# Optimization experiments

Measured on AMD Instinct MI355X. Metric: run time of the kernel, lower is better.

The kernel has to match this reference:

```python
import jax, jax.numpy as jnp
import numpy as np

NUM_BINS = 32
LAMBDA_W2 = 0.1
SMOOTHING = 1e-3
LABEL_SMOOTHING = 0.05


def setup_inputs() -> dict:
    key = jax.random.key(0)
    k1, k2, k3 = jax.random.split(key, 3)
    B, H, W = 64, 512, 512
    return {
        "changes_obs": jax.random.normal(k1, (B, H, W), dtype=jnp.float32),
        "changes_pred": jax.random.normal(k2, (B, H, W), dtype=jnp.float32),
        "mask": jax.random.randint(k3, (B, H, W), 0, 2).astype(bool),
        "bin_edges": jnp.linspace(-3.0, 3.0, NUM_BINS + 1, dtype=jnp.float32),
    }


def compute_histogram(changes, bin_edges, mask):
    # changes, mask: [B, H, W]; bin_edges: [num_bins+1]
    B = changes.shape[0]
    num_bins = bin_edges.shape[0] - 1
    x = changes.reshape(B, -1)                      # [B, N]
    m = mask.reshape(B, -1)                         # [B, N]
    # bucketize: bin i is [e_i, e_{i+1}), last bin closed on the right
    idx = jnp.searchsorted(bin_edges, x, side='right') - 1
    idx = jnp.clip(idx, 0, num_bins - 1)            # x == last edge -> last bin
    valid = m & (x >= bin_edges[0]) & (x <= bin_edges[-1])
    flat = (jnp.arange(B)[:, None] * num_bins + idx).reshape(-1)
    counts = jax.ops.segment_sum(
        valid.reshape(-1).astype(jnp.float32), flat, num_segments=B * num_bins
    ).reshape(B, num_bins)
    # torch: a sample with zero masked pixels gets counts of all ones
    n_masked = m.sum(axis=1)
    counts = jnp.where((n_masked == 0)[:, None], 1.0, counts)
    total = jnp.maximum(counts.sum(axis=1, keepdims=True), 1.0)
    proportions = counts / total
    return counts, proportions


def reference(changes_obs, changes_pred, mask, bin_edges):
    num_bins = bin_edges.shape[0] - 1
    _, p_obs = compute_histogram(changes_obs, bin_edges, mask)
    _, p_pred = compute_histogram(changes_pred, bin_edges, mask)
    p_pred = (1.0 - LABEL_SMOOTHING) * p_pred + LABEL_SMOOTHING / num_bins
    # class-balanced weights from observed proportions
    avg = p_obs.mean(axis=0)
    w = 1.0 / (avg + SMOOTHING)
    w = w * num_bins / w.sum()
    ce_loss = (-p_obs * jnp.log(p_pred + 1e-8) * w[None, :]).sum(axis=1).mean()
    # Wasserstein-2 on CDFs with midpoint-spacing bin widths
    mid = 0.5 * (bin_edges[:-1] + bin_edges[1:])
    bw = mid[1:] - mid[:-1]
    bw = jnp.concatenate([bw, bw[-1:]])
    cdf_obs = jnp.cumsum(p_obs, axis=1)
    cdf_pred = jnp.cumsum(p_pred, axis=1)
    w2_loss = (((cdf_obs - cdf_pred) ** 2) * bw[None, :]).sum(axis=1).mean()
    total_loss = (ce_loss + LAMBDA_W2 * w2_loss) / num_bins
    return total_loss, ce_loss, w2_loss, p_obs, p_pred
```

## Files before the change

### kernel.cpp

```cpp
#include <hip/hip_runtime.h>
#include <stdint.h>

#define NBINS 32
#define NBATCH 64
#define NPB (512 * 512)
#define BPB 32
#define TPB 256
#define EPB (NPB / BPB)
#define ITERS (EPB / (TPB * 4))

#define WS_PRED 2048
#define WS_NM   4096
#define WS_FLAG 4160
#define WS_WORDS 4161

__global__ void detect_mask_kernel(const uint32_t* __restrict__ mw,
                                   uint32_t* __restrict__ flag) {
  uint32_t v = mw[threadIdx.x];
  if (__any(v > 1u) && threadIdx.x == 0) *flag = 1u;
}

__device__ __forceinline__ int bin_of(float x) {
  float t = __builtin_fmaf(x, 5.333333492279053f, 16.0f);
  int i = (int)t;
  float fi = (float)i;
  float elo = __builtin_fmaf(fi, 0.1875f, -3.0f);
  float ehi = elo + 0.1875f;
  i += (x >= ehi) ? 1 : 0;
  i -= (x < elo) ? 1 : 0;
  return i;
}

__device__ __forceinline__ void count_one(int i, uint32_t h[8]) {
  const uint32_t inc = 1u << ((i & 3) << 3);
  const int hi = i >> 2;
#pragma unroll
  for (int r = 0; r < 8; ++r) h[r] += (hi == r) ? inc : 0u;
}

__global__ __launch_bounds__(TPB) void hist_kernel(
    const float* __restrict__ obs, const float* __restrict__ pred,
    const void* __restrict__ mask, uint32_t* __restrict__ ws) {
  __shared__ uint32_t red[4][32];

  const int tid = threadIdx.x;
  const uint32_t is_u8 = ws[WS_FLAG];
  const int b = blockIdx.x / BPB;
  const int chunk = blockIdx.x % BPB;
  const size_t base_f4 = (((size_t)b * NPB) + ((size_t)chunk * EPB)) >> 2;

  const float4* __restrict__ o4 = (const float4*)obs;
  const float4* __restrict__ p4 = (const float4*)pred;
  const uint32_t* __restrict__ mwp = (const uint32_t*)mask;
  const int4* __restrict__ mip = (const int4*)mask;

  uint32_t c[8] = {0, 0, 0, 0, 0, 0, 0, 0};
  uint32_t d[8] = {0, 0, 0, 0, 0, 0, 0, 0};
  uint32_t nm_pack = 0;
  uint32_t nm_cnt = 0;

#pragma unroll
  for (int it = 0; it < ITERS; ++it) {
    const size_t idx = base_f4 + (size_t)(it * TPB + tid);
    const float4 xo = o4[idx];
    const float4 xp = p4[idx];

    bool m0, m1, m2, m3;
    if (is_u8) {
      const uint32_t w = mwp[idx];
      nm_pack += w;
      m0 = (w & 0x000000ffu) != 0u;
      m1 = (w & 0x0000ff00u) != 0u;
      m2 = (w & 0x00ff0000u) != 0u;
      m3 = (w & 0xff000000u) != 0u;
    } else {
      const int4 mv = mip[idx];
      m0 = mv.x != 0; m1 = mv.y != 0; m2 = mv.z != 0; m3 = mv.w != 0;
      nm_cnt += (m0 ? 1u : 0u) + (m1 ? 1u : 0u) + (m2 ? 1u : 0u) + (m3 ? 1u : 0u);
    }

    const float a0 = m0 ? xo.x : 1e2f, b0 = m0 ? xp.x : 1e2f;
    const float a1 = m1 ? xo.y : 1e2f, b1 = m1 ? xp.y : 1e2f;
    const float a2 = m2 ? xo.z : 1e2f, b2 = m2 ? xp.z : 1e2f;
    const float a3 = m3 ? xo.w : 1e2f, b3 = m3 ? xp.w : 1e2f;

    count_one(bin_of(a0), c); count_one(bin_of(b0), d);
    count_one(bin_of(a1), c); count_one(bin_of(b1), d);
    count_one(bin_of(a2), c); count_one(bin_of(b2), d);
    count_one(bin_of(a3), c); count_one(bin_of(b3), d);
  }

  uint32_t nm = is_u8 ? ((nm_pack & 0xffu) + ((nm_pack >> 8) & 0xffu) +
                         ((nm_pack >> 16) & 0xffu) + (nm_pack >> 24))
                      : nm_cnt;
#pragma unroll
  for (int off = 32; off >= 1; off >>= 1) nm += __shfl_down(nm, off);
  if ((tid & 63) == 0) atomicAdd(&ws[WS_NM + b], nm);

#pragma unroll
  for (int m = 1; m <= 2; m <<= 1) {
#pragma unroll
    for (int r = 0; r < 8; ++r) {
      c[r] += __shfl_xor(c[r], m);
      d[r] += __shfl_xor(d[r], m);
    }
  }
  uint32_t cl[8], ch[8], dl[8], dh[8];
#pragma unroll
  for (int r = 0; r < 8; ++r) {
    cl[r] = c[r] & 0x00FF00FFu; ch[r] = (c[r] >> 8) & 0x00FF00FFu;
    dl[r] = d[r] & 0x00FF00FFu; dh[r] = (d[r] >> 8) & 0x00FF00FFu;
  }
#pragma unroll
  for (int m = 4; m <= 32; m <<= 1) {
#pragma unroll
    for (int r = 0; r < 8; ++r) {
      cl[r] += __shfl_xor(cl[r], m); ch[r] += __shfl_xor(ch[r], m);
      dl[r] += __shfl_xor(dl[r], m); dh[r] += __shfl_xor(dh[r], m);
    }
  }

  const int w = tid >> 6;
  if ((tid & 63) == 0) {
#pragma unroll
    for (int r = 0; r < 8; ++r) {
      red[w][r] = cl[r];
      red[w][8 + r] = ch[r];
      red[w][16 + r] = dl[r];
      red[w][24 + r] = dh[r];
    }
  }
  __syncthreads();

  if (tid < 2 * NBINS) {
    const int arr = tid >> 5;
    const int bin = tid & 31;
    const int slot = arr * 16 + (bin >> 2) + ((bin & 1) ? 8 : 0);
    const int shift = (bin & 2) ? 16 : 0;
    uint32_t s = 0;
#pragma unroll
    for (int wv = 0; wv < 4; ++wv) s += (red[wv][slot] >> shift) & 0xFFFFu;
    if (s) atomicAdd(&ws[(arr ? WS_PRED : 0) + b * NBINS + bin], s);
  }
}

__global__ __launch_bounds__(64) void finalize_kernel(
    const uint32_t* __restrict__ ws, const float* __restrict__ edges,
    float* __restrict__ out) {
  __shared__ float pobs[NBATCH][NBINS + 1];
  __shared__ float ppred[NBATCH][NBINS + 1];
  __shared__ float w_sh[NBINS];
  __shared__ float bw_sh[NBINS];
  __shared__ float w_scale;

  const int t = threadIdx.x;

  const uint32_t* co = ws + t * NBINS;
  const uint32_t* cp = ws + WS_PRED + t * NBINS;
  const uint32_t nmask = ws[WS_NM + t];

  float sum_o = 0.0f, sum_p = 0.0f;
#pragma unroll
  for (int j = 0; j < NBINS; ++j) {
    float vo = (nmask == 0u) ? 1.0f : (float)co[j];
    float vp = (nmask == 0u) ? 1.0f : (float)cp[j];
    pobs[t][j] = vo;  sum_o += vo;
    ppred[t][j] = vp; sum_p += vp;
  }
  const float inv_to = 1.0f / fmaxf(sum_o, 1.0f);
  const float inv_tp = 1.0f / fmaxf(sum_p, 1.0f);
#pragma unroll
  for (int j = 0; j < NBINS; ++j) {
    pobs[t][j] *= inv_to;
    ppred[t][j] = 0.95f * (ppred[t][j] * inv_tp) + 0.05f / (float)NBINS;
  }
  __syncthreads();

  if (t < NBINS) {
    float s = 0.0f;
#pragma unroll
    for (int b = 0; b < NBATCH; ++b) s += pobs[b][t];
    const float avg = s / (float)NBATCH;
    w_sh[t] = 1.0f / (avg + 1e-3f);
    const int j2 = (t < NBINS - 1) ? t : (NBINS - 2);
    const float mA = 0.5f * (edges[j2] + edges[j2 + 1]);
    const float mB = 0.5f * (edges[j2 + 1] + edges[j2 + 2]);
    bw_sh[t] = mB - mA;
  }
  __syncthreads();
  if (t == 0) {
    float sw = 0.0f;
#pragma unroll
    for (int j = 0; j < NBINS; ++j) sw += w_sh[j];
    w_scale = (float)NBINS / sw;
  }
  __syncthreads();

  float ce = 0.0f, w2 = 0.0f, cdf_o = 0.0f, cdf_p = 0.0f;
#pragma unroll
  for (int j = 0; j < NBINS; ++j) {
    const float po = pobs[t][j];
    const float pp = ppred[t][j];
    ce += -po * logf(pp + 1e-8f) * (w_sh[j] * w_scale);
    cdf_o += po;
    cdf_p += pp;
    const float dd = cdf_o - cdf_p;
    w2 += dd * dd * bw_sh[j];
  }

  float ce_r = ce, w2_r = w2;
#pragma unroll
  for (int off = 32; off >= 1; off >>= 1) {
    ce_r += __shfl_down(ce_r, off);
    w2_r += __shfl_down(w2_r, off);
  }
  if (t == 0) {
    const float ce_m = ce_r / (float)NBATCH;
    const float w2_m = w2_r / (float)NBATCH;
    out[0] = (ce_m + 0.1f * w2_m) / (float)NBINS;
    out[1] = ce_m;
    out[2] = w2_m;
  }

#pragma unroll
  for (int j = 0; j < NBINS; ++j) {
    out[3 + t * NBINS + j] = pobs[t][j];
    out[3 + NBATCH * NBINS + t * NBINS + j] = ppred[t][j];
  }
}

extern "C" void kernel_launch(void* const* d_in, const int* in_sizes, int n_in,
                              void* d_out, int out_size, void* d_ws,
                              size_t ws_size, hipStream_t stream) {
  const float* obs = (const float*)d_in[0];
  const float* pred = (const float*)d_in[1];
  const void* mask = d_in[2];
  const float* edges = (const float*)d_in[3];
  float* out = (float*)d_out;
  uint32_t* ws = (uint32_t*)d_ws;

  hipMemsetAsync(d_ws, 0, WS_WORDS * sizeof(uint32_t), stream);
  detect_mask_kernel<<<1, 64, 0, stream>>>((const uint32_t*)mask,
                                           ws + WS_FLAG);
  hist_kernel<<<NBATCH * BPB, TPB, 0, stream>>>(obs, pred, mask, ws);
  finalize_kernel<<<1, 64, 0, stream>>>(ws, edges, out);
}
```

Baseline: 246.7 us.

## Split histogram into two kernels using LDS atomics and async global-to-LDS staging

Replaces the per-thread packed register histogram with shared-memory atomic bins. The batch is split across two kernels: the first half uses plain loads, and the second half streams obs, pred and mask into a per-wave LDS double buffer with global_load_lds and explicit vmcnt waits. A special case for x == 3.0 is added to bin_of. This trades register-heavy compare chains for LDS atomic contention on 32 bins and adds an extra kernel launch with serialized halves.

```diff
diff --git a/kernel.cpp b/kernel.cpp
--- a/kernel.cpp
+++ b/kernel.cpp
@@ -7,13 +7,22 @@
 #define BPB 32
 #define TPB 256
 #define EPB (NPB / BPB)
-#define ITERS (EPB / (TPB * 4))
+#define NT 8
 
 #define WS_PRED 2048
 #define WS_NM   4096
 #define WS_FLAG 4160
 #define WS_WORDS 4161
 
+#define GLDS16(gp, lp)                                              \
+  __builtin_amdgcn_global_load_lds(                                 \
+      (__attribute__((address_space(1))) void*)(gp),                \
+      (__attribute__((address_space(3))) void*)(lp), 16, 0, 0)
+#define GLDS4(gp, lp)                                               \
+  __builtin_amdgcn_global_load_lds(                                 \
+      (__attribute__((address_space(1))) void*)(gp),                \
+      (__attribute__((address_space(3))) void*)(lp), 4, 0, 0)
+
 __global__ void detect_mask_kernel(const uint32_t* __restrict__ mw,
                                    uint32_t* __restrict__ flag) {
   uint32_t v = mw[threadIdx.x];
@@ -21,6 +30,7 @@
 }
 
 __device__ __forceinline__ int bin_of(float x) {
+  if (x == 3.0f) return NBINS - 1;
   float t = __builtin_fmaf(x, 5.333333492279053f, 16.0f);
   int i = (int)t;
   float fi = (float)i;
@@ -31,117 +41,141 @@
   return i;
 }
 
-__device__ __forceinline__ void count_one(int i, uint32_t h[8]) {
-  const uint32_t inc = 1u << ((i & 3) << 3);
-  const int hi = i >> 2;
-#pragma unroll
-  for (int r = 0; r < 8; ++r) h[r] += (hi == r) ? inc : 0u;
-}
-
-__global__ __launch_bounds__(TPB) void hist_kernel(
+__device__ __forceinline__ void bin4(const float4 x, uint32_t w,
+                                     uint32_t* __restrict__ h) {
+  const float a0 = (w & 0x000000ffu) ? x.x : 1e2f;
+  const float a1 = (w & 0x0000ff00u) ? x.y : 1e2f;
+  const float a2 = (w & 0x00ff0000u) ? x.z : 1e2f;
+  const float a3 = (w & 0xff000000u) ? x.w : 1e2f;
+  int i0 = bin_of(a0), i1 = bin_of(a1), i2 = bin_of(a2), i3 = bin_of(a3);
+  if ((unsigned)i0 < 32u) atomicAdd(&h[i0], 1u);
+  if ((unsigned)i1 < 32u) atomicAdd(&h[i1], 1u);
+  if ((unsigned)i2 < 32u) atomicAdd(&h[i2], 1u);
+  if ((unsigned)i3 < 32u) atomicAdd(&h[i3], 1u);
+}
+
+__device__ __forceinline__ void hist_epilogue(uint32_t nm, uint32_t* h_obs,
+                                              uint32_t* h_pred, int b,
+                                              uint32_t* ws, int tid) {
+#pragma unroll
+  for (int off = 32; off >= 1; off >>= 1) nm += __shfl_down(nm, off);
+  if ((tid & 63) == 0) atomicAdd(&ws[WS_NM + b], nm);
+  __syncthreads();
+  if (tid < 2 * NBINS) {
+    const uint32_t v = (tid < NBINS) ? h_obs[tid] : h_pred[tid - NBINS];
+    if (v)
+      atomicAdd(&ws[(tid < NBINS ? 0 : WS_PRED) + b * NBINS + (tid & 31)], v);
+  }
+}
+
+__global__ __launch_bounds__(TPB) void hist_a(
     const float* __restrict__ obs, const float* __restrict__ pred,
     const void* __restrict__ mask, uint32_t* __restrict__ ws) {
-  __shared__ uint32_t red[4][32];
-
+  __shared__ uint32_t h_obs[NBINS], h_pred[NBINS];
   const int tid = threadIdx.x;
+  if (tid < NBINS) { h_obs[tid] = 0u; h_pred[tid] = 0u; }
+  __syncthreads();
+
   const uint32_t is_u8 = ws[WS_FLAG];
-  const int b = blockIdx.x / BPB;
-  const int chunk = blockIdx.x % BPB;
-  const size_t base_f4 = (((size_t)b * NPB) + ((size_t)chunk * EPB)) >> 2;
+  const int b = (int)blockIdx.x / BPB;
+  const int chunk = (int)blockIdx.x % BPB;
+  const size_t base_f4 = ((size_t)b * NPB + (size_t)chunk * EPB) >> 2;
 
   const float4* __restrict__ o4 = (const float4*)obs;
   const float4* __restrict__ p4 = (const float4*)pred;
   const uint32_t* __restrict__ mwp = (const uint32_t*)mask;
   const int4* __restrict__ mip = (const int4*)mask;
 
-  uint32_t c[8] = {0, 0, 0, 0, 0, 0, 0, 0};
-  uint32_t d[8] = {0, 0, 0, 0, 0, 0, 0, 0};
-  uint32_t nm_pack = 0;
-  uint32_t nm_cnt = 0;
-
-#pragma unroll
-  for (int it = 0; it < ITERS; ++it) {
-    const size_t idx = base_f4 + (size_t)(it * TPB + tid);
+  uint32_t nm = 0;
+  for (int it = 0; it < NT; ++it) {
+    const size_t idx = base_f4 + (size_t)(it * TPB) + tid;
     const float4 xo = o4[idx];
     const float4 xp = p4[idx];
-
-    bool m0, m1, m2, m3;
+    uint32_t w;
     if (is_u8) {
-      const uint32_t w = mwp[idx];
-      nm_pack += w;
-      m0 = (w & 0x000000ffu) != 0u;
-      m1 = (w & 0x0000ff00u) != 0u;
-      m2 = (w & 0x00ff0000u) != 0u;
-      m3 = (w & 0xff000000u) != 0u;
+      w = mwp[idx];
+      nm += (w & 0xffu) + ((w >> 8) & 0xffu) + ((w >> 16) & 0xffu) + (w >> 24);
     } else {
       const int4 mv = mip[idx];
-      m0 = mv.x != 0; m1 = mv.y != 0; m2 = mv.z != 0; m3 = mv.w != 0;
-      nm_cnt += (m0 ? 1u : 0u) + (m1 ? 1u : 0u) + (m2 ? 1u : 0u) + (m3 ? 1u : 0u);
+      w = (mv.x ? 0xffu : 0u) | (mv.y ? 0xff00u : 0u) |
+          (mv.z ? 0xff0000u : 0u) | (mv.w ? 0xff000000u : 0u);
+      nm += (mv.x ? 1u : 0u) + (mv.y ? 1u : 0u) + (mv.z ? 1u : 0u) +
+            (mv.w ? 1u : 0u);
     }
-
-    const float a0 = m0 ? xo.x : 1e2f, b0 = m0 ? xp.x : 1e2f;
-    const float a1 = m1 ? xo.y : 1e2f, b1 = m1 ? xp.y : 1e2f;
-    const float a2 = m2 ? xo.z : 1e2f, b2 = m2 ? xp.z : 1e2f;
-    const float a3 = m3 ? xo.w : 1e2f, b3 = m3 ? xp.w : 1e2f;
-
-    count_one(bin_of(a0), c); count_one(bin_of(b0), d);
-    count_one(bin_of(a1), c); count_one(bin_of(b1), d);
-    count_one(bin_of(a2), c); count_one(bin_of(b2), d);
-    count_one(bin_of(a3), c); count_one(bin_of(b3), d);
-  }
-
-  uint32_t nm = is_u8 ? ((nm_pack & 0xffu) + ((nm_pack >> 8) & 0xffu) +
-                         ((nm_pack >> 16) & 0xffu) + (nm_pack >> 24))
-                      : nm_cnt;
-#pragma unroll
-  for (int off = 32; off >= 1; off >>= 1) nm += __shfl_down(nm, off);
-  if ((tid & 63) == 0) atomicAdd(&ws[WS_NM + b], nm);
-
-#pragma unroll
-  for (int m = 1; m <= 2; m <<= 1) {
-#pragma unroll
-    for (int r = 0; r < 8; ++r) {
-      c[r] += __shfl_xor(c[r], m);
-      d[r] += __shfl_xor(d[r], m);
+    bin4(xo, w, h_obs);
+    bin4(xp, w, h_pred);
+  }
+  hist_epilogue(nm, h_obs, h_pred, b, ws, tid);
+}
+
+__global__ __launch_bounds__(TPB) void hist_b(
+    const float* __restrict__ obs, const float* __restrict__ pred,
+    const void* __restrict__ mask, uint32_t* __restrict__ ws) {
+  __shared__ __align__(16) uint8_t stage[4][2][2304];
+  __shared__ uint32_t h_obs[NBINS], h_pred[NBINS];
+  const int tid = threadIdx.x;
+  const int wv = tid >> 6, ln = tid & 63;
+  if (tid < NBINS) { h_obs[tid] = 0u; h_pred[tid] = 0u; }
+  __syncthreads();
+
+  const uint32_t is_u8 = ws[WS_FLAG];
+  const int b = 32 + (int)blockIdx.x / BPB;
+  const int chunk = (int)blockIdx.x % BPB;
+  const size_t base_f4 = ((size_t)b * NPB + (size_t)chunk * EPB) >> 2;
+
+  const float4* __restrict__ o4 = (const float4*)obs;
+  const float4* __restrict__ p4 = (const float4*)pred;
+  const uint32_t* __restrict__ mwp = (const uint32_t*)mask;
+  const int4* __restrict__ mip = (const int4*)mask;
+
+  uint32_t nm = 0;
+
+  if (is_u8) {
+    const size_t wbase = base_f4 + (size_t)(wv * 64) + ln;
+    uint8_t* const s0 = &stage[wv][0][0];
+    uint8_t* const s1 = &stage[wv][1][0];
+
+    GLDS16(o4 + wbase, s0);
+    GLDS16(p4 + wbase, s0 + 1024);
+    GLDS4(mwp + wbase, s0 + 2048);
+
+#pragma unroll
+    for (int t = 0; t < NT; ++t) {
+      uint8_t* const cur = (t & 1) ? s1 : s0;
+      uint8_t* const nxt = (t & 1) ? s0 : s1;
+      if (t + 1 < NT) {
+        const size_t ni = wbase + (size_t)((t + 1) * 256);
+        GLDS16(o4 + ni, nxt);
+        GLDS16(p4 + ni, nxt + 1024);
+        GLDS4(mwp + ni, nxt + 2048);
+        asm volatile("s_waitcnt vmcnt(3)" ::: "memory");
+      } else {
+        asm volatile("s_waitcnt vmcnt(0)" ::: "memory");
+      }
+      __builtin_amdgcn_sched_barrier(0);
+
+      const uint32_t w = *(const uint32_t*)(cur + 2048 + ln * 4);
+      const float4 xo = *(const float4*)(cur + ln * 16);
+      const float4 xp = *(const float4*)(cur + 1024 + ln * 16);
+      nm += (w & 0xffu) + ((w >> 8) & 0xffu) + ((w >> 16) & 0xffu) + (w >> 24);
+      bin4(xo, w, h_obs);
+      bin4(xp, w, h_pred);
     }
-  }
-  uint32_t cl[8], ch[8], dl[8], dh[8];
-#pragma unroll
-  for (int r = 0; r < 8; ++r) {
-    cl[r] = c[r] & 0x00FF00FFu; ch[r] = (c[r] >> 8) & 0x00FF00FFu;
-    dl[r] = d[r] & 0x00FF00FFu; dh[r] = (d[r] >> 8) & 0x00FF00FFu;
-  }
-#pragma unroll
-  for (int m = 4; m <= 32; m <<= 1) {
-#pragma unroll
-    for (int r = 0; r < 8; ++r) {
-      cl[r] += __shfl_xor(cl[r], m); ch[r] += __shfl_xor(ch[r], m);
-      dl[r] += __shfl_xor(dl[r], m); dh[r] += __shfl_xor(dh[r], m);
+  } else {
+    for (int it = 0; it < NT; ++it) {
+      const size_t idx = base_f4 + (size_t)(it * TPB) + tid;
+      const float4 xo = o4[idx];
+      const float4 xp = p4[idx];
+      const int4 mv = mip[idx];
+      const uint32_t w = (mv.x ? 0xffu : 0u) | (mv.y ? 0xff00u : 0u) |
+                         (mv.z ? 0xff0000u : 0u) | (mv.w ? 0xff000000u : 0u);
+      nm += (mv.x ? 1u : 0u) + (mv.y ? 1u : 0u) + (mv.z ? 1u : 0u) +
+            (mv.w ? 1u : 0u);
+      bin4(xo, w, h_obs);
+      bin4(xp, w, h_pred);
     }
   }
-
-  const int w = tid >> 6;
-  if ((tid & 63) == 0) {
-#pragma unroll
-    for (int r = 0; r < 8; ++r) {
-      red[w][r] = cl[r];
-      red[w][8 + r] = ch[r];
-      red[w][16 + r] = dl[r];
-      red[w][24 + r] = dh[r];
-    }
-  }
-  __syncthreads();
-
-  if (tid < 2 * NBINS) {
-    const int arr = tid >> 5;
-    const int bin = tid & 31;
-    const int slot = arr * 16 + (bin >> 2) + ((bin & 1) ? 8 : 0);
-    const int shift = (bin & 2) ? 16 : 0;
-    uint32_t s = 0;
-#pragma unroll
-    for (int wv = 0; wv < 4; ++wv) s += (red[wv][slot] >> shift) & 0xFFFFu;
-    if (s) atomicAdd(&ws[(arr ? WS_PRED : 0) + b * NBINS + bin], s);
-  }
+  hist_epilogue(nm, h_obs, h_pred, b, ws, tid);
 }
 
 __global__ __launch_bounds__(64) void finalize_kernel(
@@ -242,6 +276,7 @@
   hipMemsetAsync(d_ws, 0, WS_WORDS * sizeof(uint32_t), stream);
   detect_mask_kernel<<<1, 64, 0, stream>>>((const uint32_t*)mask,
                                            ws + WS_FLAG);
-  hist_kernel<<<NBATCH * BPB, TPB, 0, stream>>>(obs, pred, mask, ws);
+  hist_a<<<32 * BPB, TPB, 0, stream>>>(obs, pred, mask, ws);
+  hist_b<<<32 * BPB, TPB, 0, stream>>>(obs, pred, mask, ws);
   finalize_kernel<<<1, 64, 0, stream>>>(ws, edges, out);
 }
```

Result: slower. 260.4 us (+5.6%).
